# Kernel tuning notes

Measured on AMD Instinct MI355X. Metric: run time of the kernel, lower is better.

The kernel has to match this reference:

```python
import jax, jax.numpy as jnp
import numpy as np

P = 7              # output_size (7,7)
SCALE = 0.125      # spatial_scale
B, C, H, W = 4, 256, 128, 128
K = 512
IMG = H / SCALE    # 1024 px image space


def setup_inputs() -> dict:
    key = jax.random.key(0)
    k1, k2, k3, k4 = jax.random.split(key, 4)
    inputs = jax.random.normal(k1, (B, C, H, W), dtype=jnp.float32)
    # rois: [K,5] = (batch_idx, x1, y1, x2, y2) in image coordinates
    bidx = jax.random.randint(k2, (K, 1), 0, B).astype(jnp.float32)
    xy = jax.random.uniform(k3, (K, 4), minval=0.0, maxval=IMG, dtype=jnp.float32)
    x1 = jnp.minimum(xy[:, 0], xy[:, 2])
    x2 = jnp.clip(jnp.maximum(xy[:, 0], xy[:, 2]), x1 + 8.0, IMG)
    y1 = jnp.minimum(xy[:, 1], xy[:, 3])
    y2 = jnp.clip(jnp.maximum(xy[:, 1], xy[:, 3]), y1 + 8.0, IMG)
    rois = jnp.stack([bidx[:, 0], x1, y1, x2, y2], axis=1)
    # per-ROI binary spatial mask over the feature map (pixel used iff > 0.5)
    masks = (jax.random.uniform(k4, (K, H, W)) > 0.2).astype(jnp.float32)
    return {"inputs": inputs, "rois": rois, "masks": masks}


def reference(inputs, rois, masks):
    Hh, Ww = inputs.shape[2], inputs.shape[3]
    hr = jnp.arange(Hh)
    wr = jnp.arange(Ww)
    pr = jnp.arange(P)
    neg = -jnp.inf

    def pool_one(args):
        roi, mask = args
        b = roi[0].astype(jnp.int32)
        f = jax.lax.dynamic_index_in_dim(inputs, b, 0, keepdims=False)  # [C,H,W]
        # torchvision-style rounded ROI bounds in feature-map coords
        sw = jnp.round(roi[1] * SCALE).astype(jnp.int32)
        sh = jnp.round(roi[2] * SCALE).astype(jnp.int32)
        ew = jnp.round(roi[3] * SCALE).astype(jnp.int32)
        eh = jnp.round(roi[4] * SCALE).astype(jnp.int32)
        roi_w = jnp.maximum(ew - sw + 1, 1)
        roi_h = jnp.maximum(eh - sh + 1, 1)
        # per-output-bin [start,end) row/col ranges (floor/ceil adaptive bins)
        hs = jnp.clip((pr * roi_h) // P + sh, 0, Hh)
        he = jnp.clip(((pr + 1) * roi_h + P - 1) // P + sh, 0, Hh)
        ws = jnp.clip((pr * roi_w) // P + sw, 0, Ww)
        we = jnp.clip(((pr + 1) * roi_w + P - 1) // P + sw, 0, Ww)
        rowmask = (hr[None, :] >= hs[:, None]) & (hr[None, :] < he[:, None])  # [P,H]
        colmask = (wr[None, :] >= ws[:, None]) & (wr[None, :] < we[:, None])  # [P,W]
        fm = jnp.where(mask > 0.5, f, neg)                                   # [C,H,W]
        # separable max: rows first, then cols (bins are rectangles)
        m1 = jnp.max(jnp.where(rowmask[:, None, :, None], fm[None], neg), axis=2)      # [P,C,W]
        m2 = jnp.max(jnp.where(colmask[None, :, None, :], m1[:, None], neg), axis=3)   # [Ph,Pw,C]
        out = jnp.where(jnp.isinf(m2), 0.0, m2)  # empty / fully-masked bin -> 0
        return jnp.transpose(out, (2, 0, 1))     # [C,P,P]

    return jax.lax.map(pool_one, (rois, masks))  # [K,C,P,P]
```

## Files before the change

### kernel.cpp

```cpp
#include <hip/hip_runtime.h>
#include <math.h>

#define P 7
#define SCALE 0.125f
#define BB 4
#define CC 256
#define HH 128
#define WW 128
#define KK 512
#define NBIN 49
#define GPB 13
#define NXCD 8

typedef unsigned short ushort8 __attribute__((ext_vector_type(8)));

__device__ __forceinline__ unsigned short f32_to_bf16_rne(float f) {
    unsigned int u = __float_as_uint(f);
    u += 0x7FFFu + ((u >> 16) & 1u);
    return (unsigned short)(u >> 16);
}

__global__ __launch_bounds__(1024) void transpose_cvt(
    const float* __restrict__ in, unsigned short* __restrict__ out)
{
    __shared__ float tile[64][65];
    const int p0 = blockIdx.x * 64;
    const int c0 = blockIdx.y * 64;
    const int b  = blockIdx.z;
    const int tx = threadIdx.x;
    const int ty = threadIdx.y;

    const float* src = in + (size_t)b * CC * (HH * WW);
#pragma unroll
    for (int j = 0; j < 64; j += 16)
        tile[ty + j][tx] =
            __builtin_nontemporal_load(&src[(size_t)(c0 + ty + j) * (HH * WW) + p0 + tx]);
    __syncthreads();

    unsigned int* dst = (unsigned int*)(out + (size_t)b * (HH * WW) * CC);
    const int t = ty * 64 + tx;
#pragma unroll
    for (int i = 0; i < 2; ++i) {
        const int flat = i * 1024 + t;
        const int px = flat >> 5;
        const int cp = flat & 31;
        const unsigned int lo = f32_to_bf16_rne(tile[cp * 2][px]);
        const unsigned int hi = f32_to_bf16_rne(tile[cp * 2 + 1][px]);
        dst[((size_t)(p0 + px) * CC + c0) / 2 + cp] = lo | (hi << 16);
    }
}

__global__ __launch_bounds__(256) void pool_bf16(
    const unsigned short* __restrict__ fT,
    const float* __restrict__ rois,
    const float* __restrict__ masks,
    float* __restrict__ out)
{
    const int pid = blockIdx.x;
    const int x   = pid & (NXCD - 1);
    const int t   = pid >> 3;
    const int g   = t % GPB;
    const int q   = t / GPB;
    const int k   = q * NXCD + x;

    const int wv   = threadIdx.x >> 6;
    const int lane = threadIdx.x & 63;
    const int bi   = g * 4 + wv;
    if (bi >= NBIN) return;
    const int ph = bi / P;
    const int pw = bi % P;

    const int half = lane >> 5;
    const int c8   = (lane & 31) * 8;

    const float* roi = rois + k * 5;
    const int b  = (int)roi[0];
    const int sw = (int)rintf(roi[1] * SCALE);
    const int sh = (int)rintf(roi[2] * SCALE);
    const int ew = (int)rintf(roi[3] * SCALE);
    const int eh = (int)rintf(roi[4] * SCALE);
    const int roi_w = max(ew - sw + 1, 1);
    const int roi_h = max(eh - sh + 1, 1);

    const int hs = min(max((ph * roi_h) / P + sh, 0), HH);
    const int he = min(max(((ph + 1) * roi_h + P - 1) / P + sh, 0), HH);
    const int wl = min(max((pw * roi_w) / P + sw, 0), WW);
    const int wr = min(max(((pw + 1) * roi_w + P - 1) / P + sw, 0), WW);

    const unsigned short* fb = fT + (size_t)b * (HH * WW) * CC;
    const float* m = masks + (size_t)k * (HH * WW);

    const float NEG = -INFINITY;
    float acc[8];
#pragma unroll
    for (int j = 0; j < 8; ++j) acc[j] = NEG;

    for (int h = hs; h < he; ++h) {
        const float* mrow = m + h * WW;
        const unsigned short* frow = fb + (size_t)h * WW * CC + c8;
#pragma unroll 2
        for (int w = wl; w < wr; w += 2) {
            const int wp = w + half;
            const bool valid = wp < wr;
            const int wc = min(wp, WW - 1);
            const float mv = mrow[wc];
            const ushort8 bits = *(const ushort8*)(frow + (size_t)wc * CC);
            const bool on = valid && (mv > 0.5f);
#pragma unroll
            for (int j = 0; j < 8; ++j) {
                const float fv = __uint_as_float(((unsigned int)bits[j]) << 16);
                acc[j] = fmaxf(acc[j], on ? fv : NEG);
            }
        }
    }

#pragma unroll
    for (int j = 0; j < 8; ++j)
        acc[j] = fmaxf(acc[j], __shfl_xor(acc[j], 32, 64));

    if (half == 0) {
        float* o = out + ((size_t)k * CC + c8) * NBIN + ph * P + pw;
#pragma unroll
        for (int j = 0; j < 8; ++j)
            o[(size_t)j * NBIN] = isinf(acc[j]) ? 0.0f : acc[j];
    }
}

__global__ __launch_bounds__(256) void ROIPool_nchw_kernel(
    const float* __restrict__ inputs, const float* __restrict__ rois,
    const float* __restrict__ masks, float* __restrict__ out)
{
    const int k  = blockIdx.x;
    const int ph = blockIdx.y;
    const int c  = threadIdx.x;

    const float* roi = rois + k * 5;
    const int b  = (int)roi[0];
    const int sw = (int)rintf(roi[1] * SCALE);
    const int sh = (int)rintf(roi[2] * SCALE);
    const int ew = (int)rintf(roi[3] * SCALE);
    const int eh = (int)rintf(roi[4] * SCALE);
    const int roi_w = max(ew - sw + 1, 1);
    const int roi_h = max(eh - sh + 1, 1);

    const int hs = min(max((ph * roi_h) / P + sh, 0), HH);
    const int he = min(max(((ph + 1) * roi_h + P - 1) / P + sh, 0), HH);

    int wsb[P], web[P];
#pragma unroll
    for (int pw = 0; pw < P; ++pw) {
        wsb[pw] = min(max((pw * roi_w) / P + sw, 0), WW);
        web[pw] = min(max(((pw + 1) * roi_w + P - 1) / P + sw, 0), WW);
    }

    const float* f = inputs + ((size_t)b * CC + c) * (HH * WW);
    const float* m = masks  + (size_t)k * (HH * WW);

    float vmax[P];
#pragma unroll
    for (int pw = 0; pw < P; ++pw) vmax[pw] = -INFINITY;

    for (int h = hs; h < he; ++h) {
        const float* frow = f + h * WW;
        const float* mrow = m + h * WW;
#pragma unroll
        for (int pw = 0; pw < P; ++pw) {
            float v = vmax[pw];
            for (int w = wsb[pw]; w < web[pw]; ++w)
                if (mrow[w] > 0.5f) v = fmaxf(v, frow[w]);
            vmax[pw] = v;
        }
    }

    float* o = out + (((size_t)k * CC + c) * P + ph) * P;
#pragma unroll
    for (int pw = 0; pw < P; ++pw) {
        const float v = vmax[pw];
        o[pw] = isinf(v) ? 0.0f : v;
    }
}

extern "C" void kernel_launch(void* const* d_in, const int* in_sizes, int n_in,
                              void* d_out, int out_size, void* d_ws, size_t ws_size,
                              hipStream_t stream) {
    const float* inputs = (const float*)d_in[0];
    const float* rois   = (const float*)d_in[1];
    const float* masks  = (const float*)d_in[2];
    float* out = (float*)d_out;

    const size_t need = (size_t)BB * CC * HH * WW * sizeof(unsigned short);

    if (ws_size >= need) {
        unsigned short* fT = (unsigned short*)d_ws;
        {
            dim3 grid((HH * WW) / 64, CC / 64, BB);
            dim3 block(64, 16);
            transpose_cvt<<<grid, block, 0, stream>>>(inputs, fT);
        }
        {
            dim3 grid(KK * GPB);
            dim3 block(256);
            pool_bf16<<<grid, block, 0, stream>>>(fT, rois, masks, out);
        }
    } else {
        dim3 grid(KK, P);
        dim3 block(CC);
        ROIPool_nchw_kernel<<<grid, block, 0, stream>>>(inputs, rois, masks, out);
    }
}
```

Baseline: 126.3 us.

## Use order-preserving bf16 keys with packed u16 max and swap loop order

The transpose kernel now stores each bf16 value as a monotone unsigned 16-bit key. The pool kernel can then take the max with v_pk_max_u16 on packed pairs instead of unpacking eight values to fp32 and applying fmaxf. This cuts ALU work per loaded element, and key zero serves as the empty-bin sentinel. The loop nest is also swapped to columns outer and rows inner, which changes the memory access order. The swap may hurt locality, and keys are decoded back to float at output.

```diff
diff --git a/kernel.cpp b/kernel.cpp
--- a/kernel.cpp
+++ b/kernel.cpp
@@ -12,12 +12,20 @@
 #define GPB 13
 #define NXCD 8
 
-typedef unsigned short ushort8 __attribute__((ext_vector_type(8)));
-
 __device__ __forceinline__ unsigned short f32_to_bf16_rne(float f) {
     unsigned int u = __float_as_uint(f);
     u += 0x7FFFu + ((u >> 16) & 1u);
     return (unsigned short)(u >> 16);
+}
+
+__device__ __forceinline__ unsigned short bf16_key(unsigned short b) {
+    return (b & 0x8000u) ? (unsigned short)(~b) : (unsigned short)(b | 0x8000u);
+}
+
+__device__ __forceinline__ unsigned int pkmax_u16(unsigned int a, unsigned int b) {
+    unsigned int d;
+    asm("v_pk_max_u16 %0, %1, %2" : "=v"(d) : "v"(a), "v"(b));
+    return d;
 }
 
 __global__ __launch_bounds__(1024) void transpose_cvt(
@@ -44,13 +52,13 @@
         const int flat = i * 1024 + t;
         const int px = flat >> 5;
         const int cp = flat & 31;
-        const unsigned int lo = f32_to_bf16_rne(tile[cp * 2][px]);
-        const unsigned int hi = f32_to_bf16_rne(tile[cp * 2 + 1][px]);
+        const unsigned int lo = bf16_key(f32_to_bf16_rne(tile[cp * 2][px]));
+        const unsigned int hi = bf16_key(f32_to_bf16_rne(tile[cp * 2 + 1][px]));
         dst[((size_t)(p0 + px) * CC + c0) / 2 + cp] = lo | (hi << 16);
     }
 }
 
-__global__ __launch_bounds__(256) void pool_bf16(
+__global__ __launch_bounds__(256) void pool_key(
     const unsigned short* __restrict__ fT,
     const float* __restrict__ rois,
     const float* __restrict__ masks,
@@ -87,42 +95,52 @@
     const int wl = min(max((pw * roi_w) / P + sw, 0), WW);
     const int wr = min(max(((pw + 1) * roi_w + P - 1) / P + sw, 0), WW);
 
-    const unsigned short* fb = fT + (size_t)b * (HH * WW) * CC;
+    const unsigned int* fb =
+        (const unsigned int*)(fT + (size_t)b * (HH * WW) * CC + c8);
     const float* m = masks + (size_t)k * (HH * WW);
 
-    const float NEG = -INFINITY;
-    float acc[8];
-#pragma unroll
-    for (int j = 0; j < 8; ++j) acc[j] = NEG;
-
-    for (int h = hs; h < he; ++h) {
-        const float* mrow = m + h * WW;
-        const unsigned short* frow = fb + (size_t)h * WW * CC + c8;
+    unsigned int a0 = 0, a1 = 0, a2 = 0, a3 = 0;
+
+    for (int w = wl; w < wr; w += 2) {
+        const int wp = w + half;
+        const bool valid = wp < wr;
+        const int wc = min(wp, WW - 1);
+        const unsigned int* fcol = fb + (size_t)wc * (CC / 2);
+        const float* mcol = m + wc;
 #pragma unroll 2
-        for (int w = wl; w < wr; w += 2) {
-            const int wp = w + half;
-            const bool valid = wp < wr;
-            const int wc = min(wp, WW - 1);
-            const float mv = mrow[wc];
-            const ushort8 bits = *(const ushort8*)(frow + (size_t)wc * CC);
+        for (int h = hs; h < he; ++h) {
+            const float mv = mcol[h * WW];
+            const uint4 kv = *(const uint4*)(fcol + (size_t)h * (WW * CC / 2));
             const bool on = valid && (mv > 0.5f);
-#pragma unroll
-            for (int j = 0; j < 8; ++j) {
-                const float fv = __uint_as_float(((unsigned int)bits[j]) << 16);
-                acc[j] = fmaxf(acc[j], on ? fv : NEG);
+            a0 = pkmax_u16(a0, on ? kv.x : 0u);
+            a1 = pkmax_u16(a1, on ? kv.y : 0u);
+            a2 = pkmax_u16(a2, on ? kv.z : 0u);
+            a3 = pkmax_u16(a3, on ? kv.w : 0u);
+        }
+    }
+
+    a0 = pkmax_u16(a0, (unsigned int)__shfl_xor((int)a0, 32, 64));
+    a1 = pkmax_u16(a1, (unsigned int)__shfl_xor((int)a1, 32, 64));
+    a2 = pkmax_u16(a2, (unsigned int)__shfl_xor((int)a2, 32, 64));
+    a3 = pkmax_u16(a3, (unsigned int)__shfl_xor((int)a3, 32, 64));
+
+    if (half == 0) {
+        const unsigned int acc[4] = {a0, a1, a2, a3};
+        float* o = out + ((size_t)k * CC + c8) * NBIN + ph * P + pw;
+#pragma unroll
+        for (int j = 0; j < 8; ++j) {
+            const unsigned int d = acc[j >> 1];
+            const unsigned int key = (j & 1) ? (d >> 16) : (d & 0xFFFFu);
+            float r;
+            if (key == 0u) {
+                r = 0.0f;
+            } else {
+                const unsigned int bbits =
+                    (key & 0x8000u) ? (key ^ 0x8000u) : (~key & 0xFFFFu);
+                r = __uint_as_float(bbits << 16);
             }
-        }
-    }
-
-#pragma unroll
-    for (int j = 0; j < 8; ++j)
-        acc[j] = fmaxf(acc[j], __shfl_xor(acc[j], 32, 64));
-
-    if (half == 0) {
-        float* o = out + ((size_t)k * CC + c8) * NBIN + ph * P + pw;
-#pragma unroll
-        for (int j = 0; j < 8; ++j)
-            o[(size_t)j * NBIN] = isinf(acc[j]) ? 0.0f : acc[j];
+            o[(size_t)j * NBIN] = r;
+        }
     }
 }
 
@@ -200,7 +218,7 @@
         {
             dim3 grid(KK * GPB);
             dim3 block(256);
-            pool_bf16<<<grid, block, 0, stream>>>(fT, rois, masks, out);
+            pool_key<<<grid, block, 0, stream>>>(fT, rois, masks, out);
         }
     } else {
         dim3 grid(KK, P);
```

Measured after the change: 140.2 us. +11.0%, slower.
